# Performance work log

Hardware: AMD Instinct MI355X
Metric: run time of the kernel (lower is better)

Reference implementation:

```python
import jax, jax.numpy as jnp
import numpy as np

B, T, D, I, C, H = 8192, 128, 7, 128, 10, 64
L = 2 ** D
SUBSET = int(I * 0.8)  # feature_subset_size = 102


def setup_inputs() -> dict:
    key = jax.random.key(0)
    ks = jax.random.split(key, 7)
    x = jax.random.normal(ks[0], (B, I), dtype=jnp.float32)
    # exact feature-subset mask: SUBSET ones per (tree, depth) row
    r = jax.random.uniform(ks[1], (T, D, I))
    ranks = jnp.argsort(jnp.argsort(r, axis=-1), axis=-1)
    feature_mask = (ranks < SUBSET).astype(jnp.float32)
    thresholds = jax.random.normal(ks[2], (T, D), dtype=jnp.float32)
    leaf_outputs = jax.random.normal(ks[3], (T, L, C), dtype=jnp.float32)
    W1 = jax.random.normal(ks[4], (I, H), dtype=jnp.float32) * 0.08
    b1 = jnp.zeros((H,), dtype=jnp.float32)
    W2 = jax.random.normal(ks[5], (H, T), dtype=jnp.float32) * 0.12
    b2 = jnp.zeros((T,), dtype=jnp.float32)
    return {"x": x, "feature_mask": feature_mask, "thresholds": thresholds,
            "leaf_outputs": leaf_outputs, "W1": W1, "b1": b1, "W2": W2, "b2": b2}


def reference(x, feature_mask, thresholds, leaf_outputs, W1, b1, W2, b2):
    depth = thresholds.shape[1]
    # split logits: masked feature sum minus threshold, per (batch, tree, depth)
    z = jnp.einsum('bi,tdi->btd', x, feature_mask) - thresholds[None, :, :]
    s = 0.5 * (z / (1.0 + jnp.abs(z)) + 1.0)  # scaled softsign split in (0,1)
    # probabilistic path routing: doubling concat, identical to torch loop
    p = jnp.ones((x.shape[0], feature_mask.shape[0], 1), dtype=x.dtype)
    for d in range(depth):
        sd = s[:, :, d:d + 1]            # [B, T, 1]
        p = jnp.concatenate([p * sd, p * (1.0 - sd)], axis=-1)  # [B, T, 2^(d+1)]
    leaf_probs = jax.nn.softmax(leaf_outputs, axis=-1)           # [T, L, C]
    tree_outputs = jnp.einsum('btl,tlc->btc', p, leaf_probs)     # [B, T, C]
    # instance-wise attention over trees (eval mode: no dropout)
    attn = jax.nn.softmax(jax.nn.relu(x @ W1 + b1) @ W2 + b2, axis=-1)  # [B, T]
    return jnp.sum(tree_outputs * attn[:, :, None], axis=1)     # [B, C]
```

## Files before the change

kernel.cpp:

```cpp
#include <hip/hip_runtime.h>
#include <hip/hip_bf16.h>
#include <hip/hip_fp16.h>


#define BB 8192
#define TT 128
#define II 128
#define CC 10
#define HH 64

#define OFF_S   0
#define OFF_LPB 4194304
#define OFF_PT  4456448

typedef __attribute__((ext_vector_type(8))) short short8;
typedef __attribute__((ext_vector_type(16))) float floatx16;

static __device__ inline unsigned int pkbf(float lo, float hi) {
  __hip_bfloat162 h = __float22bfloat162_rn(make_float2(lo, hi));
  unsigned int u;
  __builtin_memcpy(&u, &h, 4);
  return u;
}

static __device__ inline unsigned int pkh(float lo, float hi) {
  __half2 h = __float22half2_rn(make_float2(lo, hi));
  unsigned int u;
  __builtin_memcpy(&u, &h, 4);
  return u;
}

static __device__ inline short8 cvt8(float4 a, float4 b) {
  union { short8 v; unsigned int u[4]; } r;
  r.u[0] = pkbf(a.x, a.y);
  r.u[1] = pkbf(a.z, a.w);
  r.u[2] = pkbf(b.x, b.y);
  r.u[3] = pkbf(b.z, b.w);
  return r.v;
}

__global__ __launch_bounds__(256, 2) void phase1_kernel(
    const float* __restrict__ x, const float* __restrict__ mask,
    const float* __restrict__ thr, const float* __restrict__ lo,
    const float* __restrict__ W1, const float* __restrict__ b1,
    const float* __restrict__ W2, const float* __restrict__ b2,
    __half* __restrict__ sPack, unsigned int* __restrict__ lpb) {
  __shared__ float smem[8704];
  const int blk = blockIdx.x;
  const int tid = threadIdx.x;
  const int wv = tid >> 6, lane = tid & 63;
  const int half = lane >> 5, l31 = lane & 31;

  if (blk < 64) {
    const int b0 = blk * 128 + wv * 32;

    short8 axf[8];
    const float* xrow = x + (size_t)(b0 + l31) * II + half * 8;
#pragma unroll
    for (int s = 0; s < 8; ++s)
      axf[s] = cvt8(*(const float4*)(xrow + s * 16),
                    *(const float4*)(xrow + s * 16 + 4));

    floatx16 acch[2];
#pragma unroll
    for (int i = 0; i < 16; ++i) { acch[0][i] = 0.f; acch[1][i] = 0.f; }
#pragma unroll
    for (int s = 0; s < 8; ++s) {
#pragma unroll
      for (int tile = 0; tile < 2; ++tile) {
        union { short8 v; unsigned int u[4]; } wf;
#pragma unroll
        for (int jp = 0; jp < 4; ++jp) {
          int k0 = s * 16 + half * 8 + jp * 2;
          float f0 = W1[(size_t)k0 * HH + tile * 32 + l31];
          float f1 = W1[(size_t)(k0 + 1) * HH + tile * 32 + l31];
          wf.u[jp] = pkbf(f0, f1);
        }
        acch[tile] = __builtin_amdgcn_mfma_f32_32x32x16_bf16(
            axf[s], wf.v, acch[tile], 0, 0, 0);
      }
    }
    float* hids = smem + wv * 2176;
#pragma unroll
    for (int tile = 0; tile < 2; ++tile) {
      float bh = b1[tile * 32 + l31];
#pragma unroll
      for (int r = 0; r < 16; ++r) {
        int row = (r & 3) + 8 * (r >> 2) + 4 * half;
        hids[row * 68 + tile * 32 + l31] = fmaxf(acch[tile][r] + bh, 0.f);
      }
    }
    __syncthreads();

    short8 ahf[4];
#pragma unroll
    for (int s = 0; s < 4; ++s) {
      const float* hr = hids + l31 * 68 + s * 16 + half * 8;
      ahf[s] = cvt8(*(const float4*)hr, *(const float4*)(hr + 4));
    }

    floatx16 accl[4];
#pragma unroll
    for (int tile = 0; tile < 4; ++tile) {
#pragma unroll
      for (int i = 0; i < 16; ++i) accl[tile][i] = 0.f;
#pragma unroll
      for (int s = 0; s < 4; ++s) {
        union { short8 v; unsigned int u[4]; } wf;
#pragma unroll
        for (int jp = 0; jp < 4; ++jp) {
          int k0 = s * 16 + half * 8 + jp * 2;
          float f0 = W2[(size_t)k0 * TT + tile * 32 + l31];
          float f1 = W2[(size_t)(k0 + 1) * TT + tile * 32 + l31];
          wf.u[jp] = pkbf(f0, f1);
        }
        accl[tile] = __builtin_amdgcn_mfma_f32_32x32x16_bf16(
            ahf[s], wf.v, accl[tile], 0, 0, 0);
      }
      float bt = b2[tile * 32 + l31];
#pragma unroll
      for (int i = 0; i < 16; ++i) accl[tile][i] += bt;
    }

    float mrow[16];
#pragma unroll
    for (int r = 0; r < 16; ++r)
      mrow[r] = fmaxf(fmaxf(accl[0][r], accl[1][r]),
                      fmaxf(accl[2][r], accl[3][r]));
#pragma unroll
    for (int msk = 1; msk <= 16; msk <<= 1)
#pragma unroll
      for (int r = 0; r < 16; ++r)
        mrow[r] = fmaxf(mrow[r], __shfl_xor(mrow[r], msk, 64));
    float srow[16];
#pragma unroll
    for (int r = 0; r < 16; ++r) srow[r] = 0.f;
#pragma unroll
    for (int tile = 0; tile < 4; ++tile)
#pragma unroll
      for (int r = 0; r < 16; ++r) {
        float e = __expf(accl[tile][r] - mrow[r]);
        accl[tile][r] = e;
        srow[r] += e;
      }
#pragma unroll
    for (int msk = 1; msk <= 16; msk <<= 1)
#pragma unroll
      for (int r = 0; r < 16; ++r)
        srow[r] += __shfl_xor(srow[r], msk, 64);
#pragma unroll
    for (int r = 0; r < 16; ++r) srow[r] = 1.f / srow[r];

#pragma unroll
    for (int tile = 0; tile < 4; ++tile)
#pragma unroll
      for (int r = 0; r < 16; ++r) {
        int row = (r & 3) + 8 * (r >> 2) + 4 * half;
        sPack[((size_t)(tile * 32 + l31) * BB + (b0 + row)) * 8 + 7] =
            __float2half(accl[tile][r] * srow[r]);
      }

  } else if (blk < 960) {
    const int blk2 = blk - 64;
    const int mb = blk2 >> 5;
    const int ns = blk2 & 31;
    const int m0 = mb * 32;

    short8 af[8];
    const float* mrow = mask + (size_t)(m0 + l31) * II + half * 8;
#pragma unroll
    for (int s = 0; s < 8; ++s)
      af[s] = cvt8(*(const float4*)(mrow + s * 16),
                   *(const float4*)(mrow + s * 16 + 4));
    float th[16];
#pragma unroll
    for (int r = 0; r < 16; ++r)
      th[r] = thr[m0 + (r & 3) + 8 * (r >> 2) + 4 * half];

#pragma unroll
    for (int nb = 0; nb < 2; ++nb) {
      const int n0 = ns * 256 + wv * 64 + nb * 32;
      const float* xrow = x + (size_t)(n0 + l31) * II + half * 8;
      floatx16 acc;
#pragma unroll
      for (int i = 0; i < 16; ++i) acc[i] = 0.f;
#pragma unroll
      for (int s = 0; s < 8; ++s) {
        short8 bf = cvt8(*(const float4*)(xrow + s * 16),
                         *(const float4*)(xrow + s * 16 + 4));
        acc = __builtin_amdgcn_mfma_f32_32x32x16_bf16(af[s], bf, acc, 0, 0, 0);
      }
      const int b = n0 + l31;
#pragma unroll
      for (int r = 0; r < 16; ++r) {
        int row = (r & 3) + 8 * (r >> 2) + 4 * half;
        int m = m0 + row;
        int t = (m * 9363) >> 16;
        int d = m - t * 7;
        float z = acc[r] - th[r];
        float o = 0.5f * (z / (1.f + fabsf(z)) + 1.f);
        sPack[((size_t)t * BB + b) * 8 + d] = __float2half(o);
      }
    }

  } else {
    float* lps = smem;
    const int t0 = (blk - 960) * 2;
    {
      int tl = tid >> 7, l = tid & 127;
      const float* row = lo + ((size_t)(t0 + tl) * 128 + l) * CC;
      float v[CC];
      float m = -1e30f;
#pragma unroll
      for (int c = 0; c < CC; ++c) { v[c] = row[c]; m = fmaxf(m, v[c]); }
      float s = 0.f;
#pragma unroll
      for (int c = 0; c < CC; ++c) { v[c] = __expf(v[c] - m); s += v[c]; }
      float inv = 1.f / s;
      float* o = lps + (tl * 128 + l) * 12;
#pragma unroll
      for (int c = 0; c < CC; ++c) o[c] = v[c] * inv;
      o[10] = 0.f; o[11] = 0.f;
    }
    __syncthreads();

#pragma unroll
    for (int jj = 0; jj < 4; ++jj) {
      int idx = tid + 256 * jj;
      int tl = idx >> 9, rem = idx & 511;
      int s = rem >> 6, ln = rem & 63;
      int hf = ln >> 5, n = ln & 31;
      unsigned int wd[4];
#pragma unroll
      for (int jp = 0; jp < 4; ++jp) {
        int l0 = s * 16 + hf * 8 + jp * 2;
        float f0 = (n < CC) ? lps[(tl * 128 + l0) * 12 + n] : 0.f;
        float f1 = (n < CC) ? lps[(tl * 128 + l0 + 1) * 12 + n] : 0.f;
        wd[jp] = pkh(f0, f1);
      }
      ((uint4*)lpb)[(size_t)(t0 + tl) * 512 + s * 64 + ln] =
          make_uint4(wd[0], wd[1], wd[2], wd[3]);
    }
  }
}

__global__ __launch_bounds__(256, 4) void main_kernel(
    const __half* __restrict__ sPack, const unsigned int* __restrict__ lpb,
    float* __restrict__ partial) {
  __shared__ float red[128 * 10];
  const int bg = blockIdx.x, tg = blockIdx.y;
  const int tid = threadIdx.x;
  const int w = tid >> 6, lane = tid & 63;
  const int half = lane >> 5;
  const int b = bg * 128 + w * 32 + (lane & 31);
  const uint4* spk = (const uint4*)sPack;

  floatx16 acc;
#pragma unroll
  for (int i = 0; i < 16; ++i) acc[i] = 0.f;

  uint4 sv[2];
  sv[0] = spk[(size_t)(tg * 8) * BB + b];

#pragma unroll
  for (int it = 0; it < 8; ++it) {
    const int cur = it & 1;
    const int t = tg * 8 + it;
    uint4 bf[8];
    const uint4* lpt = (const uint4*)lpb + (size_t)t * 512 + lane;
#pragma unroll
    for (int s = 0; s < 8; ++s) bf[s] = lpt[s * 64];
    if (it < 7) sv[cur ^ 1] = spk[(size_t)(t + 1) * BB + b];

    const __half* sh = (const __half*)&sv[cur];
    float s0 = __half2float(sh[0]), s1 = __half2float(sh[1]);
    float s2 = __half2float(sh[2]), s3 = __half2float(sh[3]);
    float s4 = __half2float(sh[4]), s5 = __half2float(sh[5]);
    float s6 = __half2float(sh[6]), A  = __half2float(sh[7]);

    float s0c = 1.f - s0, s1c = 1.f - s1, s2c = 1.f - s2;
    float t0 = s0 * s1, t1 = s0c * s1, t2 = s0 * s1c, t3 = s0c * s1c;
    float pl[8];
    pl[0] = t0 * s2;  pl[1] = t1 * s2;  pl[2] = t2 * s2;  pl[3] = t3 * s2;
    pl[4] = t0 * s2c; pl[5] = t1 * s2c; pl[6] = t2 * s2c; pl[7] = t3 * s2c;
    float sel3 = half ? (1.f - s3) : s3;
    float Af = A * sel3;
    float s4c = 1.f - s4, s5c = 1.f - s5;
    float as6 = Af * s6, as6c = Af * (1.f - s6);
    float u0 = s4 * s5, u1 = s4c * s5, u2 = s4 * s5c, u3 = s4c * s5c;
    float wv[8];
    wv[0] = u0 * as6;  wv[1] = u1 * as6;  wv[2] = u2 * as6;  wv[3] = u3 * as6;
    wv[4] = u0 * as6c; wv[5] = u1 * as6c; wv[6] = u2 * as6c; wv[7] = u3 * as6c;

    __half2 pl2[4];
#pragma unroll
    for (int jp = 0; jp < 4; ++jp)
      pl2[jp] = __float22half2_rn(make_float2(pl[jp * 2], pl[jp * 2 + 1]));

#pragma unroll
    for (int s = 0; s < 8; ++s) {
      __half2 w2 = __half2half2(__float2half(wv[s]));
      union { short8 v; __half2 h[4]; } a;
#pragma unroll
      for (int jp = 0; jp < 4; ++jp) a.h[jp] = __hmul2(pl2[jp], w2);
      acc = __builtin_amdgcn_mfma_f32_32x32x16_f16(
          a.v, *(const short8*)&bf[s], acc, 0, 0, 0);
    }
  }

  const int col = lane & 31;
  if (col < CC) {
#pragma unroll
    for (int r = 0; r < 16; ++r) {
      int row = (r & 3) + 8 * (r >> 2) + 4 * half;
      red[(w * 32 + row) * 10 + col] = acc[r];
    }
  }
  __syncthreads();
#pragma unroll
  for (int j = 0; j < 5; ++j) {
    int idx = tid + 256 * j;
    partial[(size_t)tg * 81920 + (size_t)bg * 1280 + idx] = red[idx];
  }
}

__global__ __launch_bounds__(256) void reduce_kernel(
    const float* __restrict__ partial, float* __restrict__ out) {
  int idx = blockIdx.x * 256 + threadIdx.x;
  float s = 0.f;
#pragma unroll
  for (int tg = 0; tg < 16; ++tg) s += partial[(size_t)tg * 81920 + idx];
  out[idx] = s;
}

extern "C" void kernel_launch(void* const* d_in, const int* in_sizes, int n_in,
                              void* d_out, int out_size, void* d_ws, size_t ws_size,
                              hipStream_t stream) {
  const float* x    = (const float*)d_in[0];
  const float* mask = (const float*)d_in[1];
  const float* thr  = (const float*)d_in[2];
  const float* lo   = (const float*)d_in[3];
  const float* W1   = (const float*)d_in[4];
  const float* b1   = (const float*)d_in[5];
  const float* W2   = (const float*)d_in[6];
  const float* b2   = (const float*)d_in[7];
  float* out = (float*)d_out;
  float* ws  = (float*)d_ws;

  __half*       sPack   = (__half*)(ws + OFF_S);
  unsigned int* LPb     = (unsigned int*)(ws + OFF_LPB);
  float*        partial = ws + OFF_PT;

  phase1_kernel<<<1024, 256, 0, stream>>>(x, mask, thr, lo, W1, b1, W2, b2,
                                          sPack, LPb);
  main_kernel<<<dim3(64, 16), 256, 0, stream>>>(sPack, LPb, partial);
  reduce_kernel<<<320, 256, 0, stream>>>(partial, out);
}
```

Measured before the change: 124.4 us.

## Write split probabilities coalesced, then repack into per-tree packed layout

```diff
diff --git a/kernel.cpp b/kernel.cpp
--- a/kernel.cpp
+++ b/kernel.cpp
@@ -9,9 +9,11 @@
 #define CC 10
 #define HH 64
 
-#define OFF_S   0
-#define OFF_LPB 4194304
-#define OFF_PT  4456448
+#define OFF_STH 0
+#define OFF_AT  3670016
+#define OFF_SP  4194304
+#define OFF_LPB 8388608
+#define OFF_PT  8650752
 
 typedef __attribute__((ext_vector_type(8))) short short8;
 typedef __attribute__((ext_vector_type(16))) float floatx16;
@@ -44,7 +46,8 @@
     const float* __restrict__ thr, const float* __restrict__ lo,
     const float* __restrict__ W1, const float* __restrict__ b1,
     const float* __restrict__ W2, const float* __restrict__ b2,
-    __half* __restrict__ sPack, unsigned int* __restrict__ lpb) {
+    __half* __restrict__ sTh, __half* __restrict__ attnB,
+    unsigned int* __restrict__ lpb) {
   __shared__ float smem[8704];
   const int blk = blockIdx.x;
   const int tid = threadIdx.x;
@@ -156,7 +159,7 @@
 #pragma unroll
       for (int r = 0; r < 16; ++r) {
         int row = (r & 3) + 8 * (r >> 2) + 4 * half;
-        sPack[((size_t)(tile * 32 + l31) * BB + (b0 + row)) * 8 + 7] =
+        attnB[(size_t)(b0 + row) * TT + tile * 32 + l31] =
             __float2half(accl[tile][r] * srow[r]);
       }
 
@@ -190,16 +193,12 @@
                          *(const float4*)(xrow + s * 16 + 4));
         acc = __builtin_amdgcn_mfma_f32_32x32x16_bf16(af[s], bf, acc, 0, 0, 0);
       }
-      const int b = n0 + l31;
 #pragma unroll
       for (int r = 0; r < 16; ++r) {
         int row = (r & 3) + 8 * (r >> 2) + 4 * half;
-        int m = m0 + row;
-        int t = (m * 9363) >> 16;
-        int d = m - t * 7;
         float z = acc[r] - th[r];
         float o = 0.5f * (z / (1.f + fabsf(z)) + 1.f);
-        sPack[((size_t)t * BB + b) * 8 + d] = __float2half(o);
+        sTh[(size_t)(m0 + row) * BB + n0 + l31] = __float2half(o);
       }
     }
 
@@ -244,9 +243,22 @@
   }
 }
 
+__global__ __launch_bounds__(256) void repack_kernel(
+    const __half* __restrict__ sTh, __half* __restrict__ sPack) {
+  int idx = blockIdx.x * 256 + threadIdx.x;
+  int b = idx & (BB - 1);
+  int t = idx >> 13;
+  union { uint4 v; __half h[8]; } p;
+#pragma unroll
+  for (int d = 0; d < 7; ++d)
+    p.h[d] = sTh[(size_t)(t * 7 + d) * BB + b];
+  p.h[7] = __float2half(0.f);
+  ((uint4*)sPack)[(size_t)t * BB + b] = p.v;
+}
+
 __global__ __launch_bounds__(256, 4) void main_kernel(
-    const __half* __restrict__ sPack, const unsigned int* __restrict__ lpb,
-    float* __restrict__ partial) {
+    const __half* __restrict__ sPack, const __half* __restrict__ attnB,
+    const unsigned int* __restrict__ lpb, float* __restrict__ partial) {
   __shared__ float red[128 * 10];
   const int bg = blockIdx.x, tg = blockIdx.y;
   const int tid = threadIdx.x;
@@ -255,6 +267,9 @@
   const int b = bg * 128 + w * 32 + (lane & 31);
   const uint4* spk = (const uint4*)sPack;
 
+  __half av[8];
+  *(uint4*)av = *(const uint4*)(attnB + (size_t)b * TT + tg * 8);
+
   floatx16 acc;
 #pragma unroll
   for (int i = 0; i < 16; ++i) acc[i] = 0.f;
@@ -276,7 +291,8 @@
     float s0 = __half2float(sh[0]), s1 = __half2float(sh[1]);
     float s2 = __half2float(sh[2]), s3 = __half2float(sh[3]);
     float s4 = __half2float(sh[4]), s5 = __half2float(sh[5]);
-    float s6 = __half2float(sh[6]), A  = __half2float(sh[7]);
+    float s6 = __half2float(sh[6]);
+    float A  = __half2float(av[it]);
 
     float s0c = 1.f - s0, s1c = 1.f - s1, s2c = 1.f - s2;
     float t0 = s0 * s1, t1 = s0c * s1, t2 = s0 * s1c, t3 = s0c * s1c;
@@ -347,12 +363,15 @@
   float* out = (float*)d_out;
   float* ws  = (float*)d_ws;
 
-  __half*       sPack   = (__half*)(ws + OFF_S);
+  __half*       sTh     = (__half*)(ws + OFF_STH);
+  __half*       attnB   = (__half*)(ws + OFF_AT);
+  __half*       sPack   = (__half*)(ws + OFF_SP);
   unsigned int* LPb     = (unsigned int*)(ws + OFF_LPB);
   float*        partial = ws + OFF_PT;
 
   phase1_kernel<<<1024, 256, 0, stream>>>(x, mask, thr, lo, W1, b1, W2, b2,
-                                          sPack, LPb);
-  main_kernel<<<dim3(64, 16), 256, 0, stream>>>(sPack, LPb, partial);
+                                          sTh, attnB, LPb);
+  repack_kernel<<<4096, 256, 0, stream>>>(sTh, sPack);
+  main_kernel<<<dim3(64, 16), 256, 0, stream>>>(sPack, attnB, LPb, partial);
   reduce_kernel<<<320, 256, 0, stream>>>(partial, out);
 }
```

Result: faster. 118.3 us (-4.9%).
